# Optimization experiments

Measured on AMD Instinct MI355X. Metric: run time of the kernel, lower is better.

Reference implementation:

```python
import jax, jax.numpy as jnp
import numpy as np

N_NODES = 20000
N_EDGES = 320000
IN_C = 256
HID = 32
HEADS0 = 4  # n_heads[0]: both #modules in first layer and heads per module
OUT_C = 40
NEG_SLOPE = 0.2


def _segment_softmax(e, seg, n):
    # e: [E, H], softmax over edges grouped by destination node
    m = jax.ops.segment_max(e, seg, num_segments=n)
    m = jnp.where(jnp.isfinite(m), m, 0.0)  # nodes with no in-edges
    ex = jnp.exp(e - m[seg])
    s = jax.ops.segment_sum(ex, seg, num_segments=n)
    return ex / (s[seg] + 1e-16)


def _gat_conv(x, W, a_src, a_dst, bias, src, dst, n, concat):
    # PyG GATConv math (self-loops assumed already appended to src/dst)
    H, C = a_src.shape
    h = (x @ W).reshape(n, H, C)                      # [N, H, C]
    e_src = (h * a_src).sum(-1)                       # [N, H]
    e_dst = (h * a_dst).sum(-1)                       # [N, H]
    e = jax.nn.leaky_relu(e_src[src] + e_dst[dst], NEG_SLOPE)  # [E, H]
    alpha = _segment_softmax(e, dst, n)               # [E, H]
    out = jax.ops.segment_sum(h[src] * alpha[:, :, None], dst, num_segments=n)
    if concat:
        return out.reshape(n, H * C) + bias
    return out.mean(axis=1) + bias


def setup_inputs() -> dict:
    key = jax.random.key(0)
    ks = jax.random.split(key, 12)
    x = jax.random.normal(ks[0], (N_NODES, IN_C), dtype=jnp.float32)
    edge_index = jax.random.randint(ks[1], (2, N_EDGES), 0, N_NODES, dtype=jnp.int32)
    M = HEADS0  # number of first-layer modules
    W1 = jax.random.normal(ks[2], (M, IN_C, HEADS0 * HID), dtype=jnp.float32) * 0.1
    a_src1 = jax.random.normal(ks[3], (M, HEADS0, HID), dtype=jnp.float32) * 0.1
    a_dst1 = jax.random.normal(ks[4], (M, HEADS0, HID), dtype=jnp.float32) * 0.1
    b1 = jax.random.normal(ks[5], (M, HEADS0 * HID), dtype=jnp.float32) * 0.1
    cat_dim = M * HEADS0 * HID  # 512: actual width after torch.cat over modules
    W2 = jax.random.normal(ks[6], (cat_dim, OUT_C), dtype=jnp.float32) * 0.1
    a_src2 = jax.random.normal(ks[7], (1, OUT_C), dtype=jnp.float32) * 0.1
    a_dst2 = jax.random.normal(ks[8], (1, OUT_C), dtype=jnp.float32) * 0.1
    b2 = jax.random.normal(ks[9], (OUT_C,), dtype=jnp.float32) * 0.1
    return {"x": x, "edge_index": edge_index, "W1": W1, "a_src1": a_src1,
            "a_dst1": a_dst1, "b1": b1, "W2": W2, "a_src2": a_src2,
            "a_dst2": a_dst2, "b2": b2}


def reference(x, edge_index, W1, a_src1, a_dst1, b1, W2, a_src2, a_dst2, b2):
    n = x.shape[0]
    loops = jnp.arange(n, dtype=edge_index.dtype)  # PyG add_self_loops=True
    src = jnp.concatenate([edge_index[0], loops])
    dst = jnp.concatenate([edge_index[1], loops])
    # first layer: HEADS0 independent GATConv modules, outputs concatenated
    outs = jax.vmap(lambda W, a_s, a_d, b: _gat_conv(x, W, a_s, a_d, b, src, dst, n, True))(
        W1, a_src1, a_dst1, b1)                      # [M, N, HEADS0*HID]
    h = jnp.transpose(outs, (1, 0, 2)).reshape(n, -1)  # [N, 512]
    h = jax.nn.elu(h)  # dropout is a no-op in eval mode
    out = _gat_conv(h, W2, a_src2, a_dst2, b2, src, dst, n, False)  # [N, OUT_C]
    return jax.nn.log_softmax(out, axis=1)
```

## Files before the change

kernel.cpp:

```cpp
#include <hip/hip_runtime.h>
#include <cstdint>
#include <cstddef>

#define N_NODES 20000
#define N_EDGES 320000
#define E_TOT   340000
#define IN_C    256
#define HID     32
#define HEADS0  4
#define OUT_C   40
#define NEG_SLOPE 0.2f
#define CAT     512
#define MH      16
#define H2S     48

typedef unsigned short ushort_t;
typedef __attribute__((ext_vector_type(8))) short short8v;
typedef __attribute__((ext_vector_type(4))) float f32x4;
typedef __attribute__((ext_vector_type(8))) unsigned short ushort8v;

#define WAVE_FENCE() asm volatile("" ::: "memory")

__device__ inline float bf2f(unsigned short u) {
  union { unsigned int i; float f; } c; c.i = ((unsigned int)u) << 16; return c.f;
}
__device__ inline unsigned short f2bf(float f) {
  union { float f; unsigned int i; } c; c.f = f;
  unsigned int r = c.i + 0x7FFFu + ((c.i >> 16) & 1u);
  return (unsigned short)(r >> 16);
}


__global__ __launch_bounds__(256) void zero_k(int* deg, int* fill) {
  int i = blockIdx.x * 256 + threadIdx.x;
  if (i < N_NODES) { deg[i] = 0; fill[i] = 0; }
}

__global__ __launch_bounds__(256) void degree_k(const int* __restrict__ ei, int* __restrict__ deg) {
  int e = blockIdx.x * 256 + threadIdx.x;
  if (e >= E_TOT) return;
  int d = (e < N_EDGES) ? ei[N_EDGES + e] : (e - N_EDGES);
  atomicAdd(&deg[d], 1);
}

__global__ __launch_bounds__(1024) void scan_k(const int* __restrict__ deg, int* __restrict__ row_ptr) {
  const int C = 20;
  __shared__ int part[1024];
  int t = threadIdx.x;
  int b = t * C;
  int s = 0;
  for (int i = 0; i < C; i++) { int idx = b + i; if (idx < N_NODES) s += deg[idx]; }
  part[t] = s;
  __syncthreads();
  for (int off = 1; off < 1024; off <<= 1) {
    int v = part[t];
    int u = (t >= off) ? part[t - off] : 0;
    __syncthreads();
    part[t] = v + u;
    __syncthreads();
  }
  int run = (t > 0) ? part[t - 1] : 0;
  for (int i = 0; i < C; i++) {
    int idx = b + i;
    if (idx <= N_NODES) {
      row_ptr[idx] = run;
      if (idx < N_NODES) run += deg[idx];
    }
  }
}

__global__ __launch_bounds__(256) void scatter_k(const int* __restrict__ ei,
                                                 const int* __restrict__ row_ptr,
                                                 int* __restrict__ fill,
                                                 int* __restrict__ csr_src,
                                                 int* __restrict__ csr_dst) {
  int e = blockIdx.x * 256 + threadIdx.x;
  if (e >= E_TOT) return;
  int s, d;
  if (e < N_EDGES) { s = ei[e]; d = ei[N_EDGES + e]; }
  else             { s = e - N_EDGES; d = s; }
  int pos = row_ptr[d] + atomicAdd(&fill[d], 1);
  csr_src[pos] = s;
  csr_dst[pos] = d;
}


__global__ __launch_bounds__(256) void cvt_x_k(const float* __restrict__ x,
                                               ushort_t* __restrict__ xhi,
                                               ushort_t* __restrict__ xlo) {
  int i = blockIdx.x * 256 + threadIdx.x;
  if (i >= (N_NODES * IN_C) / 4) return;
  float4 v = ((const float4*)x)[i];
  ushort_t hi[4], lo[4];
  float vv[4] = {v.x, v.y, v.z, v.w};
#pragma unroll
  for (int k = 0; k < 4; k++) {
    ushort_t h = f2bf(vv[k]);
    hi[k] = h;
    lo[k] = f2bf(vv[k] - bf2f(h));
  }
  ((ushort4*)xhi)[i] = make_ushort4(hi[0], hi[1], hi[2], hi[3]);
  ((ushort4*)xlo)[i] = make_ushort4(lo[0], lo[1], lo[2], lo[3]);
}

__global__ __launch_bounds__(256) void pack_w_k(const float* __restrict__ W1,
                                                ushort_t* __restrict__ bhi,
                                                ushort_t* __restrict__ blo) {
  int idx = blockIdx.x * 256 + threadIdx.x;
  if (idx >= 32 * 8 * 64) return;
  int n16  = idx >> 9;
  int k32  = (idx >> 6) & 7;
  int lane = idx & 63;
  int cfull = n16 * 16 + (lane & 15);
  int m = cfull >> 7;
  int c = cfull & 127;
  int kbase = k32 * 32 + (lane >> 4) * 8;
#pragma unroll
  for (int b = 0; b < 8; b++) {
    float v = W1[((m << 8) + kbase + b) * 128 + c];
    ushort_t h = f2bf(v);
    bhi[(size_t)idx * 8 + b] = h;
    blo[(size_t)idx * 8 + b] = f2bf(v - bf2f(h));
  }
}

__global__ __launch_bounds__(256) void pack_w2_k(const float* __restrict__ W2,
                                                 ushort_t* __restrict__ bhi,
                                                 ushort_t* __restrict__ blo) {
  int idx = blockIdx.x * 256 + threadIdx.x;
  if (idx >= 3 * 16 * 64) return;
  int n16  = idx >> 10;
  int k32  = (idx >> 6) & 15;
  int lane = idx & 63;
  int n = n16 * 16 + (lane & 15);
  int kbase = k32 * 32 + (lane >> 4) * 8;
#pragma unroll
  for (int b = 0; b < 8; b++) {
    float v = (n < OUT_C) ? W2[(kbase + b) * OUT_C + n] : 0.f;
    ushort_t h = f2bf(v);
    bhi[(size_t)idx * 8 + b] = h;
    blo[(size_t)idx * 8 + b] = f2bf(v - bf2f(h));
  }
}

__global__ __launch_bounds__(256) void gemm1_mfma_k(const ushort_t* __restrict__ xhi,
                                                    const ushort_t* __restrict__ xlo,
                                                    const ushort_t* __restrict__ bhi,
                                                    const ushort_t* __restrict__ blo,
                                                    const float* __restrict__ a_src1,
                                                    const float* __restrict__ a_dst1,
                                                    ushort_t* __restrict__ h1b,
                                                    float* __restrict__ es1,
                                                    float* __restrict__ ed1) {
  int tid = threadIdx.x;
  int wave = tid >> 6, lane = tid & 63;
  int l15 = lane & 15, lhi = lane >> 4;
  int wrow = blockIdx.x * 64 + (wave & 1) * 32;
  int wcol = blockIdx.y * 128 + (wave >> 1) * 64;
  int n16base = wcol >> 4;

  f32x4 acc[2][4];
#pragma unroll
  for (int mf = 0; mf < 2; mf++)
#pragma unroll
    for (int nf = 0; nf < 4; nf++) acc[mf][nf] = (f32x4){0.f, 0.f, 0.f, 0.f};

  int arow[2];
#pragma unroll
  for (int mf = 0; mf < 2; mf++) {
    int r = wrow + mf * 16 + l15;
    arow[mf] = (r < N_NODES) ? r : (N_NODES - 1);
  }

  for (int ks = 0; ks < 8; ks++) {
    short8v ah[2], al[2];
#pragma unroll
    for (int mf = 0; mf < 2; mf++) {
      size_t off = (size_t)arow[mf] * IN_C + ks * 32 + lhi * 8;
      ah[mf] = *(const short8v*)(xhi + off);
      al[mf] = *(const short8v*)(xlo + off);
    }
    short8v bh[4], bl[4];
#pragma unroll
    for (int nf = 0; nf < 4; nf++) {
      size_t off = ((size_t)((n16base + nf) * 8 + ks) * 64 + lane) * 8;
      bh[nf] = *(const short8v*)(bhi + off);
      bl[nf] = *(const short8v*)(blo + off);
    }
#pragma unroll
    for (int mf = 0; mf < 2; mf++)
#pragma unroll
      for (int nf = 0; nf < 4; nf++) {
        acc[mf][nf] = __builtin_amdgcn_mfma_f32_16x16x32_bf16(ah[mf], bh[nf], acc[mf][nf], 0, 0, 0);
        acc[mf][nf] = __builtin_amdgcn_mfma_f32_16x16x32_bf16(ah[mf], bl[nf], acc[mf][nf], 0, 0, 0);
        acc[mf][nf] = __builtin_amdgcn_mfma_f32_16x16x32_bf16(al[mf], bh[nf], acc[mf][nf], 0, 0, 0);
      }
  }

#pragma unroll
  for (int mf = 0; mf < 2; mf++) {
    int rbase = wrow + mf * 16 + lhi * 4;
#pragma unroll
    for (int nf = 0; nf < 4; nf++) {
      int col = wcol + nf * 16 + l15;
#pragma unroll
      for (int r = 0; r < 4; r++) {
        int row = rbase + r;
        if (row < N_NODES)
          h1b[(size_t)row * CAT + col] = f2bf(acc[mf][nf][r]);
      }
    }
  }

  int mh0 = wcol >> 5;
  float as[4], ad[4];
#pragma unroll
  for (int nf = 0; nf < 4; nf++) {
    int aidx = (mh0 + (nf >> 1)) * HID + (nf & 1) * 16 + l15;
    as[nf] = a_src1[aidx];
    ad[nf] = a_dst1[aidx];
  }
#pragma unroll
  for (int mf = 0; mf < 2; mf++) {
#pragma unroll
    for (int r = 0; r < 4; r++) {
      int row = wrow + mf * 16 + lhi * 4 + r;
      float ps0 = acc[mf][0][r] * as[0] + acc[mf][1][r] * as[1];
      float ps1 = acc[mf][2][r] * as[2] + acc[mf][3][r] * as[3];
      float pd0 = acc[mf][0][r] * ad[0] + acc[mf][1][r] * ad[1];
      float pd1 = acc[mf][2][r] * ad[2] + acc[mf][3][r] * ad[3];
#pragma unroll
      for (int msk = 1; msk < 16; msk <<= 1) {
        ps0 += __shfl_xor(ps0, msk); ps1 += __shfl_xor(ps1, msk);
        pd0 += __shfl_xor(pd0, msk); pd1 += __shfl_xor(pd1, msk);
      }
      if (l15 == 0 && row < N_NODES) {
        es1[row * MH + mh0]     = ps0;
        es1[row * MH + mh0 + 1] = ps1;
        ed1[row * MH + mh0]     = pd0;
        ed1[row * MH + mh0 + 1] = pd1;
      }
    }
  }
}

__global__ __launch_bounds__(256) void escore_k(const float* __restrict__ es1,
                                                const float* __restrict__ ed1,
                                                const int* __restrict__ csr_src,
                                                const int* __restrict__ csr_dst,
                                                ushort_t* __restrict__ exq) {
  int p = blockIdx.x * 256 + threadIdx.x;
  if (p >= E_TOT) return;
  int s = csr_src[p], d = csr_dst[p];
  const float4* sp = (const float4*)(es1 + (size_t)s * MH);
  const float4* dp = (const float4*)(ed1 + (size_t)d * MH);
  float4 a0 = sp[0], a1 = sp[1], a2 = sp[2], a3 = sp[3];
  float4 b0 = dp[0], b1 = dp[1], b2 = dp[2], b3 = dp[3];
  float v[16] = {a0.x + b0.x, a0.y + b0.y, a0.z + b0.z, a0.w + b0.w,
                 a1.x + b1.x, a1.y + b1.y, a1.z + b1.z, a1.w + b1.w,
                 a2.x + b2.x, a2.y + b2.y, a2.z + b2.z, a2.w + b2.w,
                 a3.x + b3.x, a3.y + b3.y, a3.z + b3.z, a3.w + b3.w};
  ushort8v o0, o1;
#pragma unroll
  for (int i = 0; i < 16; i++) {
    float e = v[i];
    e = (e > 0.f) ? e : e * NEG_SLOPE;
    float ex = __expf(e);
    if (i < 8) o0[i] = f2bf(ex); else o1[i - 8] = f2bf(ex);
  }
  *(ushort8v*)(exq + (size_t)p * MH)     = o0;
  *(ushort8v*)(exq + (size_t)p * MH + 8) = o1;
}


__global__ __launch_bounds__(256) void agg1_k(const ushort_t* __restrict__ h1b,
                                              const ushort_t* __restrict__ exq,
                                              const int* __restrict__ row_ptr,
                                              const int* __restrict__ csr_src,
                                              const float* __restrict__ b1,
                                              ushort_t* __restrict__ hhi,
                                              ushort_t* __restrict__ hlo) {
  int w = threadIdx.x >> 6, lane = threadIdx.x & 63;
  int n = blockIdx.x * 4 + w;
  int beg = row_ptr[n];
  int deg = row_ptr[n + 1] - beg;
  int hh = lane >> 2;

  __shared__ float ex_buf[4][64][MH + 1];
  __shared__ int   src_buf[4][64];

  float s_part[MH];
#pragma unroll
  for (int i = 0; i < MH; i++) s_part[i] = 0.f;
  float acc[8];
#pragma unroll
  for (int j = 0; j < 8; j++) acc[j] = 0.f;

  for (int base = 0; base < deg; base += 64) {
    int cnt = min(64, deg - base);
    if (lane < cnt) {
      int p = beg + base + lane;
      src_buf[w][lane] = csr_src[p];
      ushort8v q0 = *(const ushort8v*)(exq + (size_t)p * MH);
      ushort8v q1 = *(const ushort8v*)(exq + (size_t)p * MH + 8);
#pragma unroll
      for (int i = 0; i < 8; i++) {
        float ex = bf2f(q0[i]);
        ex_buf[w][lane][i] = ex;
        s_part[i] += ex;
      }
#pragma unroll
      for (int i = 0; i < 8; i++) {
        float ex = bf2f(q1[i]);
        ex_buf[w][lane][8 + i] = ex;
        s_part[8 + i] += ex;
      }
    }
    WAVE_FENCE();
    int e = 0;
    for (; e + 3 < cnt; e += 4) {
      int s0 = src_buf[w][e + 0], s1 = src_buf[w][e + 1];
      int s2 = src_buf[w][e + 2], s3 = src_buf[w][e + 3];
      float x0 = ex_buf[w][e + 0][hh], x1 = ex_buf[w][e + 1][hh];
      float x2 = ex_buf[w][e + 2][hh], x3 = ex_buf[w][e + 3][hh];
      ushort8v v0 = *(const ushort8v*)(h1b + (size_t)s0 * CAT + lane * 8);
      ushort8v v1 = *(const ushort8v*)(h1b + (size_t)s1 * CAT + lane * 8);
      ushort8v v2 = *(const ushort8v*)(h1b + (size_t)s2 * CAT + lane * 8);
      ushort8v v3 = *(const ushort8v*)(h1b + (size_t)s3 * CAT + lane * 8);
#pragma unroll
      for (int j = 0; j < 8; j++) acc[j] += x0 * bf2f(v0[j]);
#pragma unroll
      for (int j = 0; j < 8; j++) acc[j] += x1 * bf2f(v1[j]);
#pragma unroll
      for (int j = 0; j < 8; j++) acc[j] += x2 * bf2f(v2[j]);
#pragma unroll
      for (int j = 0; j < 8; j++) acc[j] += x3 * bf2f(v3[j]);
    }
    for (; e < cnt; e++) {
      int s = src_buf[w][e];
      float xv = ex_buf[w][e][hh];
      ushort8v hv = *(const ushort8v*)(h1b + (size_t)s * CAT + lane * 8);
#pragma unroll
      for (int j = 0; j < 8; j++) acc[j] += xv * bf2f(hv[j]);
    }
    WAVE_FENCE();
  }

  float denom = 0.f;
#pragma unroll
  for (int i = 0; i < MH; i++) {
    float v = s_part[i];
    v += __shfl_xor(v, 1);  v += __shfl_xor(v, 2);  v += __shfl_xor(v, 4);
    v += __shfl_xor(v, 8);  v += __shfl_xor(v, 16); v += __shfl_xor(v, 32);
    if (hh == i) denom = v;
  }
  denom += 1e-16f;

  const float4* b1p = (const float4*)(b1 + lane * 8);
  float4 bq0 = b1p[0], bq1 = b1p[1];
  float bv8[8] = {bq0.x, bq0.y, bq0.z, bq0.w, bq1.x, bq1.y, bq1.z, bq1.w};

  ushort8v vhi, vlo;
#pragma unroll
  for (int j = 0; j < 8; j++) {
    float o = acc[j] / denom + bv8[j];
    float e = (o > 0.f) ? o : (__expf(o) - 1.f);
    ushort_t h = f2bf(e);
    vhi[j] = h;
    vlo[j] = f2bf(e - bf2f(h));
  }
  *(ushort8v*)(hhi + (size_t)n * CAT + lane * 8) = vhi;
  *(ushort8v*)(hlo + (size_t)n * CAT + lane * 8) = vlo;
}

__global__ __launch_bounds__(256) void gemm2_mfma_k(const ushort_t* __restrict__ hhi,
                                                    const ushort_t* __restrict__ hlo,
                                                    const ushort_t* __restrict__ b2hi,
                                                    const ushort_t* __restrict__ b2lo,
                                                    const float* __restrict__ a_src2,
                                                    const float* __restrict__ a_dst2,
                                                    float* __restrict__ h2,
                                                    float* __restrict__ es2,
                                                    float* __restrict__ ed2) {
  int tid = threadIdx.x;
  int wave = tid >> 6, lane = tid & 63;
  int l15 = lane & 15, lhi = lane >> 4;
  int wrow = blockIdx.x * 64 + wave * 16;

  f32x4 acc[3];
#pragma unroll
  for (int nf = 0; nf < 3; nf++) acc[nf] = (f32x4){0.f, 0.f, 0.f, 0.f};

  int r0 = wrow + l15;
  int arow = (r0 < N_NODES) ? r0 : (N_NODES - 1);

  for (int ks = 0; ks < 16; ks++) {
    size_t aoff = (size_t)arow * CAT + ks * 32 + lhi * 8;
    short8v ah = *(const short8v*)(hhi + aoff);
    short8v al = *(const short8v*)(hlo + aoff);
#pragma unroll
    for (int nf = 0; nf < 3; nf++) {
      size_t boff = ((size_t)(nf * 16 + ks) * 64 + lane) * 8;
      short8v bh = *(const short8v*)(b2hi + boff);
      short8v bl = *(const short8v*)(b2lo + boff);
      acc[nf] = __builtin_amdgcn_mfma_f32_16x16x32_bf16(ah, bh, acc[nf], 0, 0, 0);
      acc[nf] = __builtin_amdgcn_mfma_f32_16x16x32_bf16(ah, bl, acc[nf], 0, 0, 0);
      acc[nf] = __builtin_amdgcn_mfma_f32_16x16x32_bf16(al, bh, acc[nf], 0, 0, 0);
    }
  }

  float av[3], bv[3];
#pragma unroll
  for (int nf = 0; nf < 3; nf++) {
    int col = nf * 16 + l15;
    av[nf] = (col < OUT_C) ? a_src2[col] : 0.f;
    bv[nf] = (col < OUT_C) ? a_dst2[col] : 0.f;
  }
#pragma unroll
  for (int r = 0; r < 4; r++) {
    int row = wrow + lhi * 4 + r;
    float ps = acc[0][r] * av[0] + acc[1][r] * av[1] + acc[2][r] * av[2];
    float pd = acc[0][r] * bv[0] + acc[1][r] * bv[1] + acc[2][r] * bv[2];
    ps += __shfl_xor(ps, 1); pd += __shfl_xor(pd, 1);
    ps += __shfl_xor(ps, 2); pd += __shfl_xor(pd, 2);
    ps += __shfl_xor(ps, 4); pd += __shfl_xor(pd, 4);
    ps += __shfl_xor(ps, 8); pd += __shfl_xor(pd, 8);
    if (row < N_NODES) {
#pragma unroll
      for (int nf = 0; nf < 3; nf++)
        h2[(size_t)row * H2S + nf * 16 + l15] = acc[nf][r];
      if (l15 == 0) { es2[row] = ps; ed2[row] = pd; }
    }
  }
}

__global__ __launch_bounds__(256) void agg2_k(const float* __restrict__ h2,
                                              const float* __restrict__ es2,
                                              const float* __restrict__ ed2,
                                              const int* __restrict__ row_ptr,
                                              const int* __restrict__ csr_src,
                                              const float* __restrict__ b2,
                                              float* __restrict__ out) {
  int w = threadIdx.x >> 6, lane = threadIdx.x & 63;
  int n = blockIdx.x * 4 + w;
  int beg = row_ptr[n];
  int deg = row_ptr[n + 1] - beg;
  float edn = ed2[n];

  __shared__ float exb[4][64];
  __shared__ int   srb[4][64];

  float acc = 0.f, ssum = 0.f;
  for (int base = 0; base < deg; base += 64) {
    int cnt = min(64, deg - base);
    if (lane < cnt) {
      int s = csr_src[beg + base + lane];
      srb[w][lane] = s;
      float ev = es2[s] + edn;
      ev = (ev > 0.f) ? ev : ev * NEG_SLOPE;
      float ex = __expf(ev);
      exb[w][lane] = ex;
      ssum += ex;
    }
    WAVE_FENCE();
    int e = 0;
    for (; e + 3 < cnt; e += 4) {
      int s0 = srb[w][e], s1 = srb[w][e + 1], s2 = srb[w][e + 2], s3 = srb[w][e + 3];
      float x0 = exb[w][e], x1 = exb[w][e + 1], x2 = exb[w][e + 2], x3 = exb[w][e + 3];
      if (lane < OUT_C) {
        float v0 = h2[(size_t)s0 * H2S + lane];
        float v1 = h2[(size_t)s1 * H2S + lane];
        float v2 = h2[(size_t)s2 * H2S + lane];
        float v3 = h2[(size_t)s3 * H2S + lane];
        acc += x0 * v0; acc += x1 * v1; acc += x2 * v2; acc += x3 * v3;
      }
    }
    for (; e < cnt; e++) {
      int s = srb[w][e];
      float x = exb[w][e];
      if (lane < OUT_C) acc += x * h2[(size_t)s * H2S + lane];
    }
    WAVE_FENCE();
  }

  ssum += __shfl_xor(ssum, 1); ssum += __shfl_xor(ssum, 2); ssum += __shfl_xor(ssum, 4);
  ssum += __shfl_xor(ssum, 8); ssum += __shfl_xor(ssum, 16); ssum += __shfl_xor(ssum, 32);

  float val = (lane < OUT_C) ? (acc / (ssum + 1e-16f) + b2[lane]) : -INFINITY;

  float rmax = val;
#pragma unroll
  for (int o = 1; o < 64; o <<= 1) rmax = fmaxf(rmax, __shfl_xor(rmax, o));
  float ex = (lane < OUT_C) ? __expf(val - rmax) : 0.f;
  float sume = ex;
#pragma unroll
  for (int o = 1; o < 64; o <<= 1) sume += __shfl_xor(sume, o);
  if (lane < OUT_C) out[(size_t)n * OUT_C + lane] = val - rmax - __logf(sume);
}


extern "C" void kernel_launch(void* const* d_in, const int* in_sizes, int n_in,
                              void* d_out, int out_size, void* d_ws, size_t ws_size,
                              hipStream_t stream) {
  const float* x      = (const float*)d_in[0];
  const int*   ei     = (const int*)d_in[1];
  const float* W1     = (const float*)d_in[2];
  const float* a_src1 = (const float*)d_in[3];
  const float* a_dst1 = (const float*)d_in[4];
  const float* b1     = (const float*)d_in[5];
  const float* W2     = (const float*)d_in[6];
  const float* a_src2 = (const float*)d_in[7];
  const float* a_dst2 = (const float*)d_in[8];
  const float* b2     = (const float*)d_in[9];
  float* out = (float*)d_out;

  char* ws = (char*)d_ws;
  size_t off = 0;
  auto alloc = [&](size_t bytes) -> void* {
    void* p = ws + off;
    off += (bytes + 255) & ~(size_t)255;
    return p;
  };
  ushort_t* xhi  = (ushort_t*)alloc((size_t)N_NODES * IN_C * 2);
  ushort_t* xlo  = (ushort_t*)alloc((size_t)N_NODES * IN_C * 2);
  ushort_t* bhi  = (ushort_t*)alloc((size_t)32 * 8 * 64 * 8 * 2);
  ushort_t* blo  = (ushort_t*)alloc((size_t)32 * 8 * 64 * 8 * 2);
  ushort_t* b2hi = (ushort_t*)alloc((size_t)3 * 16 * 64 * 8 * 2);
  ushort_t* b2lo = (ushort_t*)alloc((size_t)3 * 16 * 64 * 8 * 2);
  ushort_t* h1b  = (ushort_t*)alloc((size_t)N_NODES * CAT * 2);
  ushort_t* hhi  = (ushort_t*)alloc((size_t)N_NODES * CAT * 2);
  ushort_t* hlo  = (ushort_t*)alloc((size_t)N_NODES * CAT * 2);
  float* es1     = (float*)alloc((size_t)N_NODES * MH * 4);
  float* ed1     = (float*)alloc((size_t)N_NODES * MH * 4);
  float* h2      = (float*)alloc((size_t)N_NODES * H2S * 4);
  float* es2     = (float*)alloc((size_t)N_NODES * 4);
  float* ed2     = (float*)alloc((size_t)N_NODES * 4);
  int*   deg     = (int*)alloc((size_t)N_NODES * 4);
  int*   fill    = (int*)alloc((size_t)N_NODES * 4);
  int*   row_ptr = (int*)alloc((size_t)(N_NODES + 1) * 4);
  int*   csr_src = (int*)alloc((size_t)E_TOT * 4);
  int*   csr_dst = (int*)alloc((size_t)E_TOT * 4);
  ushort_t* exq  = xhi;

  zero_k<<<(N_NODES + 255) / 256, 256, 0, stream>>>(deg, fill);
  degree_k<<<(E_TOT + 255) / 256, 256, 0, stream>>>(ei, deg);
  scan_k<<<1, 1024, 0, stream>>>(deg, row_ptr);
  scatter_k<<<(E_TOT + 255) / 256, 256, 0, stream>>>(ei, row_ptr, fill, csr_src, csr_dst);
  cvt_x_k<<<(N_NODES * IN_C / 4 + 255) / 256, 256, 0, stream>>>(x, xhi, xlo);
  pack_w_k<<<(32 * 8 * 64 + 255) / 256, 256, 0, stream>>>(W1, bhi, blo);
  pack_w2_k<<<(3 * 16 * 64 + 255) / 256, 256, 0, stream>>>(W2, b2hi, b2lo);
  gemm1_mfma_k<<<dim3((N_NODES + 63) / 64, CAT / 128), 256, 0, stream>>>(
      xhi, xlo, bhi, blo, a_src1, a_dst1, h1b, es1, ed1);
  escore_k<<<(E_TOT + 255) / 256, 256, 0, stream>>>(es1, ed1, csr_src, csr_dst, exq);
  agg1_k<<<N_NODES / 4, 256, 0, stream>>>(h1b, exq, row_ptr, csr_src, b1, hhi, hlo);
  gemm2_mfma_k<<<(N_NODES + 63) / 64, 256, 0, stream>>>(hhi, hlo, b2hi, b2lo, a_src2, a_dst2, h2, es2, ed2);
  agg2_k<<<N_NODES / 4, 256, 0, stream>>>(h2, es2, ed2, row_ptr, csr_src, b2, out);
}
```

Before: 218.6 us.

## Fuse edge scatter with score computation, merge prep kernels, store h2 as bf16

Edge scoring now happens inside the CSR scatter kernel, so the separate escore pass and the csr_dst array are gone. The three conversion and packing kernels become one prep kernel, and zero_k is replaced by a memset over both counters. The layer-2 features h2 are stored in bf16 to halve the gather traffic in agg2. This cuts kernel launches and memory traffic at some precision cost, and the scattered per-edge score writes follow atomic-ordered positions.

```diff
diff --git a/kernel.cpp b/kernel.cpp
--- a/kernel.cpp
+++ b/kernel.cpp
@@ -30,11 +30,6 @@
   return (unsigned short)(r >> 16);
 }
 
-
-__global__ __launch_bounds__(256) void zero_k(int* deg, int* fill) {
-  int i = blockIdx.x * 256 + threadIdx.x;
-  if (i < N_NODES) { deg[i] = 0; fill[i] = 0; }
-}
 
 __global__ __launch_bounds__(256) void degree_k(const int* __restrict__ ei, int* __restrict__ deg) {
   int e = blockIdx.x * 256 + threadIdx.x;
@@ -69,11 +64,13 @@
   }
 }
 
-__global__ __launch_bounds__(256) void scatter_k(const int* __restrict__ ei,
-                                                 const int* __restrict__ row_ptr,
-                                                 int* __restrict__ fill,
-                                                 int* __restrict__ csr_src,
-                                                 int* __restrict__ csr_dst) {
+__global__ __launch_bounds__(256) void scatter_score_k(const int* __restrict__ ei,
+                                                       const int* __restrict__ row_ptr,
+                                                       int* __restrict__ fill,
+                                                       int* __restrict__ csr_src,
+                                                       const float* __restrict__ es1,
+                                                       const float* __restrict__ ed1,
+                                                       ushort_t* __restrict__ exq) {
   int e = blockIdx.x * 256 + threadIdx.x;
   if (e >= E_TOT) return;
   int s, d;
@@ -81,65 +78,82 @@
   else             { s = e - N_EDGES; d = s; }
   int pos = row_ptr[d] + atomicAdd(&fill[d], 1);
   csr_src[pos] = s;
-  csr_dst[pos] = d;
-}
-
-
-__global__ __launch_bounds__(256) void cvt_x_k(const float* __restrict__ x,
-                                               ushort_t* __restrict__ xhi,
-                                               ushort_t* __restrict__ xlo) {
-  int i = blockIdx.x * 256 + threadIdx.x;
-  if (i >= (N_NODES * IN_C) / 4) return;
-  float4 v = ((const float4*)x)[i];
-  ushort_t hi[4], lo[4];
-  float vv[4] = {v.x, v.y, v.z, v.w};
-#pragma unroll
-  for (int k = 0; k < 4; k++) {
-    ushort_t h = f2bf(vv[k]);
-    hi[k] = h;
-    lo[k] = f2bf(vv[k] - bf2f(h));
-  }
-  ((ushort4*)xhi)[i] = make_ushort4(hi[0], hi[1], hi[2], hi[3]);
-  ((ushort4*)xlo)[i] = make_ushort4(lo[0], lo[1], lo[2], lo[3]);
-}
-
-__global__ __launch_bounds__(256) void pack_w_k(const float* __restrict__ W1,
-                                                ushort_t* __restrict__ bhi,
-                                                ushort_t* __restrict__ blo) {
-  int idx = blockIdx.x * 256 + threadIdx.x;
-  if (idx >= 32 * 8 * 64) return;
-  int n16  = idx >> 9;
-  int k32  = (idx >> 6) & 7;
-  int lane = idx & 63;
-  int cfull = n16 * 16 + (lane & 15);
-  int m = cfull >> 7;
-  int c = cfull & 127;
-  int kbase = k32 * 32 + (lane >> 4) * 8;
-#pragma unroll
-  for (int b = 0; b < 8; b++) {
-    float v = W1[((m << 8) + kbase + b) * 128 + c];
-    ushort_t h = f2bf(v);
-    bhi[(size_t)idx * 8 + b] = h;
-    blo[(size_t)idx * 8 + b] = f2bf(v - bf2f(h));
-  }
-}
-
-__global__ __launch_bounds__(256) void pack_w2_k(const float* __restrict__ W2,
-                                                 ushort_t* __restrict__ bhi,
-                                                 ushort_t* __restrict__ blo) {
-  int idx = blockIdx.x * 256 + threadIdx.x;
-  if (idx >= 3 * 16 * 64) return;
-  int n16  = idx >> 10;
-  int k32  = (idx >> 6) & 15;
-  int lane = idx & 63;
-  int n = n16 * 16 + (lane & 15);
-  int kbase = k32 * 32 + (lane >> 4) * 8;
-#pragma unroll
-  for (int b = 0; b < 8; b++) {
-    float v = (n < OUT_C) ? W2[(kbase + b) * OUT_C + n] : 0.f;
-    ushort_t h = f2bf(v);
-    bhi[(size_t)idx * 8 + b] = h;
-    blo[(size_t)idx * 8 + b] = f2bf(v - bf2f(h));
+
+  const float4* sp = (const float4*)(es1 + (size_t)s * MH);
+  const float4* dp = (const float4*)(ed1 + (size_t)d * MH);
+  float4 a0 = sp[0], a1 = sp[1], a2 = sp[2], a3 = sp[3];
+  float4 b0 = dp[0], b1 = dp[1], b2 = dp[2], b3 = dp[3];
+  float v[16] = {a0.x + b0.x, a0.y + b0.y, a0.z + b0.z, a0.w + b0.w,
+                 a1.x + b1.x, a1.y + b1.y, a1.z + b1.z, a1.w + b1.w,
+                 a2.x + b2.x, a2.y + b2.y, a2.z + b2.z, a2.w + b2.w,
+                 a3.x + b3.x, a3.y + b3.y, a3.z + b3.z, a3.w + b3.w};
+  ushort8v o0, o1;
+#pragma unroll
+  for (int i = 0; i < 16; i++) {
+    float ev = v[i];
+    ev = (ev > 0.f) ? ev : ev * NEG_SLOPE;
+    float ex = __expf(ev);
+    if (i < 8) o0[i] = f2bf(ex); else o1[i - 8] = f2bf(ex);
+  }
+  *(ushort8v*)(exq + (size_t)pos * MH)     = o0;
+  *(ushort8v*)(exq + (size_t)pos * MH + 8) = o1;
+}
+
+#define XB (N_NODES * IN_C / 4 / 256)
+
+__global__ __launch_bounds__(256) void prep_k(const float* __restrict__ x,
+                                              ushort_t* __restrict__ xhi,
+                                              ushort_t* __restrict__ xlo,
+                                              const float* __restrict__ W1,
+                                              ushort_t* __restrict__ bhi,
+                                              ushort_t* __restrict__ blo,
+                                              const float* __restrict__ W2,
+                                              ushort_t* __restrict__ b2hi,
+                                              ushort_t* __restrict__ b2lo) {
+  int blk = blockIdx.x;
+  if (blk < XB) {
+    int i = blk * 256 + threadIdx.x;
+    float4 v = ((const float4*)x)[i];
+    ushort_t hi[4], lo[4];
+    float vv[4] = {v.x, v.y, v.z, v.w};
+#pragma unroll
+    for (int k = 0; k < 4; k++) {
+      ushort_t h = f2bf(vv[k]);
+      hi[k] = h;
+      lo[k] = f2bf(vv[k] - bf2f(h));
+    }
+    ((ushort4*)xhi)[i] = make_ushort4(hi[0], hi[1], hi[2], hi[3]);
+    ((ushort4*)xlo)[i] = make_ushort4(lo[0], lo[1], lo[2], lo[3]);
+  } else if (blk < XB + 64) {
+    int idx = (blk - XB) * 256 + threadIdx.x;
+    int n16  = idx >> 9;
+    int k32  = (idx >> 6) & 7;
+    int lane = idx & 63;
+    int cfull = n16 * 16 + (lane & 15);
+    int m = cfull >> 7;
+    int c = cfull & 127;
+    int kbase = k32 * 32 + (lane >> 4) * 8;
+#pragma unroll
+    for (int b = 0; b < 8; b++) {
+      float v = W1[((m << 8) + kbase + b) * 128 + c];
+      ushort_t h = f2bf(v);
+      bhi[(size_t)idx * 8 + b] = h;
+      blo[(size_t)idx * 8 + b] = f2bf(v - bf2f(h));
+    }
+  } else {
+    int idx = (blk - XB - 64) * 256 + threadIdx.x;
+    int n16  = idx >> 10;
+    int k32  = (idx >> 6) & 15;
+    int lane = idx & 63;
+    int n = n16 * 16 + (lane & 15);
+    int kbase = k32 * 32 + (lane >> 4) * 8;
+#pragma unroll
+    for (int b = 0; b < 8; b++) {
+      float v = (n < OUT_C) ? W2[(kbase + b) * OUT_C + n] : 0.f;
+      ushort_t h = f2bf(v);
+      b2hi[(size_t)idx * 8 + b] = h;
+      b2lo[(size_t)idx * 8 + b] = f2bf(v - bf2f(h));
+    }
   }
 }
 
@@ -244,34 +258,6 @@
   }
 }
 
-__global__ __launch_bounds__(256) void escore_k(const float* __restrict__ es1,
-                                                const float* __restrict__ ed1,
-                                                const int* __restrict__ csr_src,
-                                                const int* __restrict__ csr_dst,
-                                                ushort_t* __restrict__ exq) {
-  int p = blockIdx.x * 256 + threadIdx.x;
-  if (p >= E_TOT) return;
-  int s = csr_src[p], d = csr_dst[p];
-  const float4* sp = (const float4*)(es1 + (size_t)s * MH);
-  const float4* dp = (const float4*)(ed1 + (size_t)d * MH);
-  float4 a0 = sp[0], a1 = sp[1], a2 = sp[2], a3 = sp[3];
-  float4 b0 = dp[0], b1 = dp[1], b2 = dp[2], b3 = dp[3];
-  float v[16] = {a0.x + b0.x, a0.y + b0.y, a0.z + b0.z, a0.w + b0.w,
-                 a1.x + b1.x, a1.y + b1.y, a1.z + b1.z, a1.w + b1.w,
-                 a2.x + b2.x, a2.y + b2.y, a2.z + b2.z, a2.w + b2.w,
-                 a3.x + b3.x, a3.y + b3.y, a3.z + b3.z, a3.w + b3.w};
-  ushort8v o0, o1;
-#pragma unroll
-  for (int i = 0; i < 16; i++) {
-    float e = v[i];
-    e = (e > 0.f) ? e : e * NEG_SLOPE;
-    float ex = __expf(e);
-    if (i < 8) o0[i] = f2bf(ex); else o1[i - 8] = f2bf(ex);
-  }
-  *(ushort8v*)(exq + (size_t)p * MH)     = o0;
-  *(ushort8v*)(exq + (size_t)p * MH + 8) = o1;
-}
-
 
 __global__ __launch_bounds__(256) void agg1_k(const ushort_t* __restrict__ h1b,
                                               const ushort_t* __restrict__ exq,
@@ -379,7 +365,7 @@
                                                     const ushort_t* __restrict__ b2lo,
                                                     const float* __restrict__ a_src2,
                                                     const float* __restrict__ a_dst2,
-                                                    float* __restrict__ h2,
+                                                    ushort_t* __restrict__ h2b,
                                                     float* __restrict__ es2,
                                                     float* __restrict__ ed2) {
   int tid = threadIdx.x;
@@ -428,13 +414,13 @@
     if (row < N_NODES) {
 #pragma unroll
       for (int nf = 0; nf < 3; nf++)
-        h2[(size_t)row * H2S + nf * 16 + l15] = acc[nf][r];
+        h2b[(size_t)row * H2S + nf * 16 + l15] = f2bf(acc[nf][r]);
       if (l15 == 0) { es2[row] = ps; ed2[row] = pd; }
     }
   }
 }
 
-__global__ __launch_bounds__(256) void agg2_k(const float* __restrict__ h2,
+__global__ __launch_bounds__(256) void agg2_k(const ushort_t* __restrict__ h2b,
                                               const float* __restrict__ es2,
                                               const float* __restrict__ ed2,
                                               const int* __restrict__ row_ptr,
@@ -468,17 +454,17 @@
       int s0 = srb[w][e], s1 = srb[w][e + 1], s2 = srb[w][e + 2], s3 = srb[w][e + 3];
       float x0 = exb[w][e], x1 = exb[w][e + 1], x2 = exb[w][e + 2], x3 = exb[w][e + 3];
       if (lane < OUT_C) {
-        float v0 = h2[(size_t)s0 * H2S + lane];
-        float v1 = h2[(size_t)s1 * H2S + lane];
-        float v2 = h2[(size_t)s2 * H2S + lane];
-        float v3 = h2[(size_t)s3 * H2S + lane];
+        float v0 = bf2f(h2b[(size_t)s0 * H2S + lane]);
+        float v1 = bf2f(h2b[(size_t)s1 * H2S + lane]);
+        float v2 = bf2f(h2b[(size_t)s2 * H2S + lane]);
+        float v3 = bf2f(h2b[(size_t)s3 * H2S + lane]);
         acc += x0 * v0; acc += x1 * v1; acc += x2 * v2; acc += x3 * v3;
       }
     }
     for (; e < cnt; e++) {
       int s = srb[w][e];
-      float x = exb[w][e];
-      if (lane < OUT_C) acc += x * h2[(size_t)s * H2S + lane];
+      float xv = exb[w][e];
+      if (lane < OUT_C) acc += xv * bf2f(h2b[(size_t)s * H2S + lane]);
     }
     WAVE_FENCE();
   }
@@ -532,27 +518,25 @@
   ushort_t* hlo  = (ushort_t*)alloc((size_t)N_NODES * CAT * 2);
   float* es1     = (float*)alloc((size_t)N_NODES * MH * 4);
   float* ed1     = (float*)alloc((size_t)N_NODES * MH * 4);
-  float* h2      = (float*)alloc((size_t)N_NODES * H2S * 4);
+  ushort_t* h2b  = (ushort_t*)alloc((size_t)N_NODES * H2S * 2);
   float* es2     = (float*)alloc((size_t)N_NODES * 4);
   float* ed2     = (float*)alloc((size_t)N_NODES * 4);
   int*   deg     = (int*)alloc((size_t)N_NODES * 4);
   int*   fill    = (int*)alloc((size_t)N_NODES * 4);
   int*   row_ptr = (int*)alloc((size_t)(N_NODES + 1) * 4);
   int*   csr_src = (int*)alloc((size_t)E_TOT * 4);
-  int*   csr_dst = (int*)alloc((size_t)E_TOT * 4);
   ushort_t* exq  = xhi;
 
-  zero_k<<<(N_NODES + 255) / 256, 256, 0, stream>>>(deg, fill);
+  hipMemsetAsync(deg, 0, ((size_t)N_NODES * 4 + 255 & ~(size_t)255) + (size_t)N_NODES * 4, stream);
+
   degree_k<<<(E_TOT + 255) / 256, 256, 0, stream>>>(ei, deg);
   scan_k<<<1, 1024, 0, stream>>>(deg, row_ptr);
-  scatter_k<<<(E_TOT + 255) / 256, 256, 0, stream>>>(ei, row_ptr, fill, csr_src, csr_dst);
-  cvt_x_k<<<(N_NODES * IN_C / 4 + 255) / 256, 256, 0, stream>>>(x, xhi, xlo);
-  pack_w_k<<<(32 * 8 * 64 + 255) / 256, 256, 0, stream>>>(W1, bhi, blo);
-  pack_w2_k<<<(3 * 16 * 64 + 255) / 256, 256, 0, stream>>>(W2, b2hi, b2lo);
+  prep_k<<<XB + 64 + 12, 256, 0, stream>>>(x, xhi, xlo, W1, bhi, blo, W2, b2hi, b2lo);
   gemm1_mfma_k<<<dim3((N_NODES + 63) / 64, CAT / 128), 256, 0, stream>>>(
       xhi, xlo, bhi, blo, a_src1, a_dst1, h1b, es1, ed1);
-  escore_k<<<(E_TOT + 255) / 256, 256, 0, stream>>>(es1, ed1, csr_src, csr_dst, exq);
+  scatter_score_k<<<(E_TOT + 255) / 256, 256, 0, stream>>>(
+      ei, row_ptr, fill, csr_src, es1, ed1, exq);
   agg1_k<<<N_NODES / 4, 256, 0, stream>>>(h1b, exq, row_ptr, csr_src, b1, hhi, hlo);
-  gemm2_mfma_k<<<(N_NODES + 63) / 64, 256, 0, stream>>>(hhi, hlo, b2hi, b2lo, a_src2, a_dst2, h2, es2, ed2);
-  agg2_k<<<N_NODES / 4, 256, 0, stream>>>(h2, es2, ed2, row_ptr, csr_src, b2, out);
-}
+  gemm2_mfma_k<<<(N_NODES + 63) / 64, 256, 0, stream>>>(hhi, hlo, b2hi, b2lo, a_src2, a_dst2, h2b, es2, ed2);
+  agg2_k<<<N_NODES / 4, 256, 0, stream>>>(h2b, es2, ed2, row_ptr, csr_src, b2, out);
+}
```

After: 207.8 us. -5.0%, faster.
